# Performance work log

Hardware: AMD Instinct MI355X
Metric: run time of the kernel (lower is better)

Reference implementation:

```python
import jax, jax.numpy as jnp
import numpy as np

D_MODEL = 1024
D_STATE = 128
EXPAND = 2
HEADDIM = 64
D_CONV = 4
VAR_NUM = 3
D_INNER = EXPAND * D_MODEL            # 2048
NHEADS = D_INNER // HEADDIM           # 32
CONV_DIM = D_INNER + 2 * D_STATE      # 2304 (x, B, C share the conv)
D_IN_PROJ = 2 * D_INNER + 2 * D_STATE + NHEADS  # 4384


def setup_inputs() -> dict:
    key = jax.random.key(0)
    ks = jax.random.split(key, 10)
    s = 0.02
    B, L = 4, 2048
    return {
        "h_prev": jax.random.normal(ks[0], (B, L, D_MODEL), jnp.float32),
        "emb_next": jax.random.normal(ks[1], (B, L, D_MODEL), jnp.float32),
        "norm_w": jnp.ones((D_MODEL,), jnp.float32),
        "proj_W": jax.random.normal(ks[2], (D_MODEL, 2 * D_MODEL), jnp.float32) * s,
        "proj_b": jnp.zeros((D_MODEL,), jnp.float32),
        "in_proj_W": jax.random.normal(ks[3], (D_IN_PROJ, D_MODEL), jnp.float32) * s,
        "conv_w": jax.random.normal(ks[4], (CONV_DIM, D_CONV), jnp.float32) * s,
        "conv_b": jnp.zeros((CONV_DIM,), jnp.float32),
        "dt_bias": jax.random.uniform(ks[5], (NHEADS,), jnp.float32) * 0.1,
        "A_log": jnp.log(jnp.arange(1, NHEADS + 1, dtype=jnp.float32)),
        "D": jnp.ones((NHEADS,), jnp.float32),
        "gnorm_w": jnp.ones((D_INNER,), jnp.float32),
        "out_proj_W": jax.random.normal(ks[6], (D_MODEL, D_INNER), jnp.float32) * s,
        "dec_W": jax.random.normal(ks[7], (VAR_NUM, D_MODEL), jnp.float32) * s,
        "dec_b": jnp.zeros((VAR_NUM,), jnp.float32),
    }


def rmsnorm(x, w, eps=1e-6):
    xf = x.astype(jnp.float32)
    v = jnp.mean(jnp.square(xf), axis=-1, keepdims=True)
    return w * (xf * jax.lax.rsqrt(v + eps)).astype(x.dtype)


def gated_rmsnorm(y, z, w, eps=1e-5):
    y = y * jax.nn.silu(z)
    v = jnp.mean(jnp.square(y.astype(jnp.float32)), axis=-1, keepdims=True)
    return w * (y.astype(jnp.float32) * jax.lax.rsqrt(v + eps)).astype(y.dtype)


def mamba2(u, in_proj_W, conv_w, conv_b, dt_bias, A_log, D, gnorm_w, out_proj_W):
    B, L, _ = u.shape
    zxbcdt = u @ in_proj_W.T  # [B,L,D_IN_PROJ]
    z, xBC, dt = jnp.split(zxbcdt, [D_INNER, D_INNER + CONV_DIM], axis=-1)
    # causal depthwise conv over time
    lhs = jnp.moveaxis(xBC, -1, 1)               # [B,C,L]
    rhs = conv_w[:, None, :]                     # [C,1,K]
    conv = jax.lax.conv_general_dilated(lhs, rhs, (1,), [(D_CONV - 1, 0)],
                                        feature_group_count=CONV_DIM)
    xBC = jax.nn.silu(jnp.moveaxis(conv, 1, -1) + conv_b)
    x, Bm, Cm = jnp.split(xBC, [D_INNER, D_INNER + D_STATE], axis=-1)
    x = x.reshape(B, L, NHEADS, HEADDIM)         # [B,L,H,P]
    dt = jax.nn.softplus(dt + dt_bias)           # [B,L,H]
    A = -jnp.exp(A_log)                          # [H]
    dA = jnp.exp(dt * A)                         # [B,L,H]

    def step(state, inp):
        dA_t, dt_t, B_t, C_t, x_t = inp          # [B,H],[B,H],[B,N],[B,N],[B,H,P]
        state = state * dA_t[..., None, None] + (dt_t[..., None, None] * x_t[..., None]) * B_t[:, None, None, :]
        y_t = jnp.einsum('bhpn,bn->bhp', state, C_t)
        return state, y_t

    init = jnp.zeros((B, NHEADS, HEADDIM, D_STATE), u.dtype)
    xs = (jnp.moveaxis(dA, 1, 0), jnp.moveaxis(dt, 1, 0), jnp.moveaxis(Bm, 1, 0),
          jnp.moveaxis(Cm, 1, 0), jnp.moveaxis(x, 1, 0))
    _, y = jax.lax.scan(step, init, xs)          # y: [L,B,H,P]
    y = jnp.moveaxis(y, 0, 1) + D[None, None, :, None] * x
    y = y.reshape(B, L, D_INNER)
    y = gated_rmsnorm(y, z, gnorm_w)
    return y @ out_proj_W.T                      # [B,L,D_MODEL]


def reference(h_prev, emb_next, norm_w, proj_W, proj_b, in_proj_W, conv_w, conv_b,
              dt_bias, A_log, D, gnorm_w, out_proj_W, dec_W, dec_b):
    combined = jnp.concatenate([rmsnorm(h_prev, norm_w), rmsnorm(emb_next, norm_w)], axis=-1)
    h_prime = combined @ proj_W.T + proj_b       # [B,L,D_MODEL]
    h_k = mamba2(h_prime, in_proj_W, conv_w, conv_b, dt_bias, A_log, D, gnorm_w, out_proj_W)
    output = h_k @ dec_W.T + dec_b               # [B,L,VAR_NUM]
    return output, h_k
```

## Files before the change

kernel.cpp:

```cpp
#include <hip/hip_runtime.h>
#include <stdint.h>

#define T_TOK 8192
#define SEQL  2048
#define DM    1024
#define DI    2048
#define DSTATE 128
#define NH    32
#define HD    64
#define CONVD 2304
#define DINP  4384
#define LD_ZX 4480
#define QC    64
#define NCH   32

typedef __attribute__((ext_vector_type(8))) __bf16 bfrag;
typedef __attribute__((ext_vector_type(8))) short s16x8;
typedef __attribute__((ext_vector_type(4))) float f32x4;

__device__ __forceinline__ float bf2f(unsigned short u){
  return __uint_as_float(((unsigned)u) << 16);
}
__device__ __forceinline__ unsigned short f2bf(float f){
  unsigned u = __float_as_uint(f);
  unsigned r = (u + 0x7FFFu + ((u >> 16) & 1u)) >> 16;
  return (unsigned short)r;
}

__device__ __forceinline__ void gl_lds16(const unsigned short* g, unsigned short* l){
  __builtin_amdgcn_global_load_lds(
      (const __attribute__((address_space(1))) void*)g,
      (__attribute__((address_space(3))) void*)l,
      16, 0, 0);
}
__device__ __forceinline__ void gl_lds4(const float* g, float* l){
  __builtin_amdgcn_global_load_lds(
      (const __attribute__((address_space(1))) void*)g,
      (__attribute__((address_space(3))) void*)l,
      4, 0, 0);
}

__global__ __launch_bounds__(256) void cvt_w_kernel(const float* __restrict__ src,
                                                    unsigned short* __restrict__ dst,
                                                    int n4, int srcn4){
  int i = blockIdx.x * 256 + threadIdx.x;
  if (i >= n4) return;
  ushort4 o;
  if (i < srcn4){
    float4 v = ((const float4*)src)[i];
    o.x = f2bf(v.x); o.y = f2bf(v.y); o.z = f2bf(v.z); o.w = f2bf(v.w);
  } else {
    o.x = o.y = o.z = o.w = 0;
  }
  *(ushort4*)(dst + (size_t)i * 4) = o;
}

__global__ __launch_bounds__(256) void rmsnorm2_kernel(const float* __restrict__ a,
                                                       const float* __restrict__ b,
                                                       const float* __restrict__ w,
                                                       unsigned short* __restrict__ out){
  int t = blockIdx.x, tid = threadIdx.x;
  float4 va = *(const float4*)(a + (size_t)t * DM + tid * 4);
  float4 vb = *(const float4*)(b + (size_t)t * DM + tid * 4);
  float sa = va.x*va.x + va.y*va.y + va.z*va.z + va.w*va.w;
  float sb = vb.x*vb.x + vb.y*vb.y + vb.z*vb.z + vb.w*vb.w;
  #pragma unroll
  for (int o = 32; o; o >>= 1){ sa += __shfl_down(sa, o); sb += __shfl_down(sb, o); }
  __shared__ float reda[4], redb[4];
  int wv = tid >> 6, lane = tid & 63;
  if (!lane){ reda[wv] = sa; redb[wv] = sb; }
  __syncthreads();
  float ta = reda[0] + reda[1] + reda[2] + reda[3];
  float tb = redb[0] + redb[1] + redb[2] + redb[3];
  float ra = rsqrtf(ta * (1.f/1024.f) + 1e-6f);
  float rb = rsqrtf(tb * (1.f/1024.f) + 1e-6f);
  float4 vw = *(const float4*)(w + tid * 4);
  unsigned short* o0 = out + (size_t)t * DI + tid * 4;
  o0[0] = f2bf(va.x*ra*vw.x); o0[1] = f2bf(va.y*ra*vw.y);
  o0[2] = f2bf(va.z*ra*vw.z); o0[3] = f2bf(va.w*ra*vw.w);
  unsigned short* o1 = o0 + DM;
  o1[0] = f2bf(vb.x*rb*vw.x); o1[1] = f2bf(vb.y*rb*vw.y);
  o1[2] = f2bf(vb.z*rb*vw.z); o1[3] = f2bf(vb.w*rb*vw.w);
}

template<bool F32OUT>
__global__ __launch_bounds__(256) void gemm_bf16_kernel(const unsigned short* __restrict__ A,
                                                        const unsigned short* __restrict__ W,
                                                        void* __restrict__ Cv,
                                                        const float* __restrict__ bias,
                                                        int M, int N, int K, int ldc){
  __shared__ unsigned short As[128 * 64];
  __shared__ unsigned short Bs[128 * 64];
  const int nN = N >> 7;
  int bid = blockIdx.x;
  const int cpx = gridDim.x >> 3;
  bid = (bid & 7) * cpx + (bid >> 3);
  const int tm = bid / nN, tn = bid % nN;
  const int tid = threadIdx.x;
  const int wv = tid >> 6, lane = tid & 63;
  const int wm = wv >> 1, wn = wv & 1;
  const int rA = lane >> 3;
  const int cA = (lane & 7) << 3;
  const size_t arow0 = (size_t)(tm * 128) * K;
  const size_t brow0 = (size_t)(tn * 128) * K;

  f32x4 zero4 = {0.f, 0.f, 0.f, 0.f};
  f32x4 acc[4][4];
  #pragma unroll
  for (int i = 0; i < 4; ++i)
    #pragma unroll
    for (int j = 0; j < 4; ++j) acc[i][j] = zero4;

  const int nK = K >> 6;
  for (int kt = 0; kt < nK; ++kt){
    const int k0 = kt << 6;
    if (kt) __syncthreads();
    #pragma unroll
    for (int i = 0; i < 4; ++i){
      int base = (wv * 4 + i) * 8;
      gl_lds16(A + arow0 + (size_t)(base + rA) * K + k0 + cA, &As[base * 64]);
      gl_lds16(W + brow0 + (size_t)(base + rA) * K + k0 + cA, &Bs[base * 64]);
    }
    __syncthreads();
    #pragma unroll
    for (int kk = 0; kk < 2; ++kk){
      const int ko = kk * 32 + (lane >> 4) * 8;
      bfrag af[4], bfv[4];
      #pragma unroll
      for (int f = 0; f < 4; ++f){
        af[f]  = *reinterpret_cast<const bfrag*>(&As[(wm*64 + f*16 + (lane & 15)) * 64 + ko]);
        bfv[f] = *reinterpret_cast<const bfrag*>(&Bs[(wn*64 + f*16 + (lane & 15)) * 64 + ko]);
      }
      #pragma unroll
      for (int fm = 0; fm < 4; ++fm)
        #pragma unroll
        for (int fn = 0; fn < 4; ++fn)
          acc[fm][fn] = __builtin_amdgcn_mfma_f32_16x16x32_bf16(af[fm], bfv[fn], acc[fm][fn], 0, 0, 0);
    }
  }
  const int r0 = (lane >> 4) * 4, ci = lane & 15;
  #pragma unroll
  for (int fm = 0; fm < 4; ++fm){
    #pragma unroll
    for (int fn = 0; fn < 4; ++fn){
      int col = tn*128 + wn*64 + fn*16 + ci;
      float bv = bias ? bias[col] : 0.f;
      #pragma unroll
      for (int r = 0; r < 4; ++r){
        int row = tm*128 + wm*64 + fm*16 + r0 + r;
        float val = acc[fm][fn][r] + bv;
        if (F32OUT) ((float*)Cv)[(size_t)row * ldc + col] = val;
        else        ((unsigned short*)Cv)[(size_t)row * ldc + col] = f2bf(val);
      }
    }
  }
}

__global__ __launch_bounds__(256) void conv_kernel(const unsigned short* __restrict__ zx,
                                                   const float* __restrict__ cw,
                                                   const float* __restrict__ cb,
                                                   unsigned short* __restrict__ xbc){
  int c = blockIdx.x * 256 + threadIdx.x;
  int tg = blockIdx.y * 8;
  int l0 = tg & (SEQL - 1);
  const unsigned short* base = zx + (size_t)tg * LD_ZX + DI + c;
  float v[11];
  #pragma unroll
  for (int i = 0; i < 11; ++i){
    int ll = l0 - 3 + i;
    v[i] = (ll >= 0) ? bf2f(base[(ptrdiff_t)(i - 3) * LD_ZX]) : 0.f;
  }
  float w0 = cw[c*4+0], w1 = cw[c*4+1], w2 = cw[c*4+2], w3 = cw[c*4+3];
  float cbv = cb[c];
  unsigned short* ob = xbc + (size_t)tg * CONVD + c;
  #pragma unroll
  for (int s = 0; s < 8; ++s){
    float acc = cbv + w0*v[s] + w1*v[s+1] + w2*v[s+2] + w3*v[s+3];
    float sv = acc / (1.f + expf(-acc));
    ob[(size_t)s * CONVD] = f2bf(sv);
  }
}

__global__ __launch_bounds__(256) void cum_kernel(const unsigned short* __restrict__ zx,
                                                  const float* __restrict__ dtbias,
                                                  const float* __restrict__ alog,
                                                  float* __restrict__ cumT,
                                                  float* __restrict__ dtT,
                                                  float* __restrict__ decayG){
  int gw = blockIdx.x * 4 + (threadIdx.x >> 6);
  int l = threadIdx.x & 63;
  int c = gw & 31, h = (gw >> 5) & 31, b = gw >> 10;
  size_t t = (size_t)b * SEQL + c * QC + l;
  float xr = bf2f(zx[t * LD_ZX + 4352 + h]) + dtbias[h];
  float dt = (xr > 20.f) ? xr : log1pf(expf(xr));
  float A = -expf(alog[h]);
  float x = dt * A;
  #pragma unroll
  for (int d = 1; d < 64; d <<= 1){
    float y = __shfl_up(x, d);
    if (l >= d) x += y;
  }
  size_t o = ((size_t)(b * NH + h)) * SEQL + c * QC + l;
  cumT[o] = x;
  dtT[o] = dt;
  float tot = __shfl(x, 63);
  if (l == 0) decayG[(b * NH + h) * NCH + c] = expf(tot);
}

__global__ __launch_bounds__(256) void chunk_dS_kernel(const unsigned short* __restrict__ xbc,
                                                       const float* __restrict__ cumT,
                                                       const float* __restrict__ dtT,
                                                       unsigned short* __restrict__ dS){
  __shared__ unsigned short Xw[64 * 64];
  __shared__ unsigned short Bt[128 * 64];
  __shared__ float cumS[64], dtS[64];
  const int blk = blockIdx.x;
  const int c = blk & 31, h = (blk >> 5) & 31, b = blk >> 10;
  const int tid = threadIdx.x;
  const int wv = tid >> 6, l = tid & 63;
  const size_t tokB = (size_t)b * SEQL + c * QC;
  const int bh = b * NH + h;

  if (wv == 0) gl_lds4(cumT + (size_t)bh * SEQL + c * QC + l, cumS);
  if (wv == 1) gl_lds4(dtT  + (size_t)bh * SEQL + c * QC + l, dtS);

  const int j = tid >> 2, g4 = tid & 3;
  const unsigned short* xsrc = xbc + (tokB + j) * CONVD + h * HD + g4 * 16;
  s16x8 x0 = *(const s16x8*)xsrc, x1 = *(const s16x8*)(xsrc + 8);
  const unsigned short* bsrc = xbc + (tokB + j) * CONVD + DI + g4 * 32;
  s16x8 b0 = *(const s16x8*)bsrc,        b1 = *(const s16x8*)(bsrc + 8);
  s16x8 b2 = *(const s16x8*)(bsrc + 16), b3 = *(const s16x8*)(bsrc + 24);
  __syncthreads();

  float wj = expf(cumS[63] - cumS[j]) * dtS[j];
  const int jh = (j >> 3), jl = (j & 7);
  #pragma unroll
  for (int e = 0; e < 8; ++e){
    int p = g4 * 16 + e;
    Xw[p * 64 + ((jh ^ (p & 7)) << 3) + jl] = f2bf(bf2f((unsigned short)x0[e]) * wj);
    int p2 = p + 8;
    Xw[p2 * 64 + ((jh ^ (p2 & 7)) << 3) + jl] = f2bf(bf2f((unsigned short)x1[e]) * wj);
  }
  #pragma unroll
  for (int e = 0; e < 8; ++e){
    int n0 = g4 * 32 + e;
    Bt[(n0     ) * 64 + ((jh ^ ((n0     ) & 7)) << 3) + jl] = (unsigned short)b0[e];
    Bt[(n0 +  8) * 64 + ((jh ^ ((n0 +  8) & 7)) << 3) + jl] = (unsigned short)b1[e];
    Bt[(n0 + 16) * 64 + ((jh ^ ((n0 + 16) & 7)) << 3) + jl] = (unsigned short)b2[e];
    Bt[(n0 + 24) * 64 + ((jh ^ ((n0 + 24) & 7)) << 3) + jl] = (unsigned short)b3[e];
  }
  __syncthreads();

  f32x4 z4 = {0.f,0.f,0.f,0.f};
  f32x4 acc[4][2];
  #pragma unroll
  for (int pt = 0; pt < 4; ++pt){ acc[pt][0] = z4; acc[pt][1] = z4; }
  #pragma unroll
  for (int ks = 0; ks < 2; ++ks){
    const int au = ((ks * 4 + (l >> 4)) ^ (l & 7));
    bfrag a[4], bb[2];
    #pragma unroll
    for (int pt = 0; pt < 4; ++pt)
      a[pt] = *(const bfrag*)&Xw[(pt * 16 + (l & 15)) * 64 + au * 8];
    #pragma unroll
    for (int nt = 0; nt < 2; ++nt)
      bb[nt] = *(const bfrag*)&Bt[((wv * 2 + nt) * 16 + (l & 15)) * 64 + au * 8];
    #pragma unroll
    for (int pt = 0; pt < 4; ++pt)
      #pragma unroll
      for (int nt = 0; nt < 2; ++nt)
        acc[pt][nt] = __builtin_amdgcn_mfma_f32_16x16x32_bf16(a[pt], bb[nt], acc[pt][nt], 0, 0, 0);
  }
  unsigned short* out = dS + ((size_t)(bh * NCH + c) * 64) * 128;
  #pragma unroll
  for (int pt = 0; pt < 4; ++pt)
    #pragma unroll
    for (int nt = 0; nt < 2; ++nt)
      #pragma unroll
      for (int r = 0; r < 4; ++r){
        int p = pt * 16 + (l >> 4) * 4 + r;
        int n = (wv * 2 + nt) * 16 + (l & 15);
        out[(size_t)p * 128 + n] = f2bf(acc[pt][nt][r]);
      }
}

__global__ __launch_bounds__(256) void chunk_state_kernel(const float* __restrict__ decayG,
                                                          unsigned short* __restrict__ dS){
  int i = blockIdx.x * 256 + threadIdx.x;
  int n = i & 127, p = (i >> 7) & 63, bh = i >> 13;
  float s = 0.f;
  #pragma unroll 4
  for (int c = 0; c < NCH; ++c){
    size_t idx = ((size_t)(bh * NCH + c) * 64 + p) * 128 + n;
    unsigned short d = dS[idx];
    dS[idx] = f2bf(s);
    s = decayG[bh * NCH + c] * s + bf2f(d);
  }
}

__global__ __launch_bounds__(256) void chunk_Y_kernel(const unsigned short* __restrict__ xbc,
                                                      const unsigned short* __restrict__ Sb,
                                                      const float* __restrict__ cumT,
                                                      const float* __restrict__ dtT,
                                                      const float* __restrict__ Dvec,
                                                      unsigned short* __restrict__ ybuf){
  __shared__ unsigned short Cs[64 * 128];
  __shared__ unsigned short Bs[64 * 128];
  __shared__ unsigned short Xt[64 * 64];
  __shared__ unsigned short Ms[64 * 64];
  __shared__ float cumS[64], dtS[64];
  const int blk = blockIdx.x;
  const int c = blk & 31, h = (blk >> 5) & 31, b = blk >> 10;
  const int tid = threadIdx.x;
  const int wv = tid >> 6, l = tid & 63;
  const size_t tokB = (size_t)b * SEQL + c * QC;
  const int bh = b * NH + h;

  #pragma unroll
  for (int kk = 0; kk < 4; ++kk){
    int k = wv * 4 + kk;
    int row = k * 4 + (l >> 4);
    int us = (l & 15) ^ (row & 7);
    gl_lds16(xbc + (tokB + row) * CONVD + 2176 + us * 8, &Cs[k * 512]);
    gl_lds16(xbc + (tokB + row) * CONVD + 2048 + us * 8, &Bs[k * 512]);
  }
  if (wv == 0) gl_lds4(cumT + (size_t)bh * SEQL + c * QC + l, cumS);
  if (wv == 1) gl_lds4(dtT  + (size_t)bh * SEQL + c * QC + l, dtS);

  {
    const int j = tid >> 2, g4 = tid & 3;
    const unsigned short* xsrc = xbc + (tokB + j) * CONVD + h * HD + g4 * 16;
    s16x8 x0 = *(const s16x8*)xsrc, x1 = *(const s16x8*)(xsrc + 8);
    const int jh = j >> 3, jl = j & 7;
    #pragma unroll
    for (int e = 0; e < 8; ++e){
      int p = g4 * 16 + e;
      Xt[p * 64 + ((jh ^ (p & 7)) << 3) + jl] = (unsigned short)x0[e];
      int p2 = p + 8;
      Xt[p2 * 64 + ((jh ^ (p2 & 7)) << 3) + jl] = (unsigned short)x1[e];
    }
  }
  __syncthreads();

  bfrag sbf[4][4];
  {
    const unsigned short* sbase = Sb + (size_t)(bh * NCH + c) * 64 * 128;
    #pragma unroll
    for (int pt = 0; pt < 4; ++pt)
      #pragma unroll
      for (int ks = 0; ks < 4; ++ks){
        int p = pt * 16 + (l & 15);
        sbf[pt][ks] = *(const bfrag*)(sbase + (size_t)p * 128 + ks * 32 + (l >> 4) * 8);
      }
  }

  f32x4 z4 = {0.f,0.f,0.f,0.f};
  f32x4 macc[4] = {z4, z4, z4, z4};
  #pragma unroll
  for (int ks = 0; ks < 4; ++ks){
    const int au = (ks * 4 + (l >> 4)) ^ (l & 7);
    bfrag ca = *(const bfrag*)&Cs[(wv * 16 + (l & 15)) * 128 + au * 8];
    #pragma unroll
    for (int jt = 0; jt < 4; ++jt){
      bfrag bb = *(const bfrag*)&Bs[(jt * 16 + (l & 15)) * 128 + au * 8];
      macc[jt] = __builtin_amdgcn_mfma_f32_16x16x32_bf16(ca, bb, macc[jt], 0, 0, 0);
    }
  }
  float cj[4], dj[4];
  #pragma unroll
  for (int jt = 0; jt < 4; ++jt){
    int jv = jt * 16 + (l & 15);
    cj[jt] = cumS[jv]; dj[jt] = dtS[jv];
  }
  float ctv[4];
  #pragma unroll
  for (int r = 0; r < 4; ++r) ctv[r] = cumS[wv * 16 + (l >> 4) * 4 + r];
  #pragma unroll
  for (int jt = 0; jt < 4; ++jt){
    int jv = jt * 16 + (l & 15);
    #pragma unroll
    for (int r = 0; r < 4; ++r){
      int tb = wv * 16 + (l >> 4) * 4 + r;
      float g = (jv <= tb) ? expf(ctv[r] - cj[jt]) * dj[jt] : 0.f;
      Ms[tb * 64 + (((jv >> 3) ^ (tb & 7)) << 3) + (jv & 7)] = f2bf(macc[jt][r] * g);
    }
  }
  f32x4 yacc[4] = {z4, z4, z4, z4};
  #pragma unroll
  for (int kj = 0; kj < 2; ++kj){
    const int au = (kj * 4 + (l >> 4)) ^ (l & 7);
    bfrag ma = *(const bfrag*)&Ms[(wv * 16 + (l & 15)) * 64 + au * 8];
    #pragma unroll
    for (int pt = 0; pt < 4; ++pt){
      bfrag wx = *(const bfrag*)&Xt[(pt * 16 + (l & 15)) * 64 + au * 8];
      yacc[pt] = __builtin_amdgcn_mfma_f32_16x16x32_bf16(ma, wx, yacc[pt], 0, 0, 0);
    }
  }
  f32x4 iacc[4] = {z4, z4, z4, z4};
  #pragma unroll
  for (int ks = 0; ks < 4; ++ks){
    const int au = (ks * 4 + (l >> 4)) ^ (l & 7);
    bfrag ca = *(const bfrag*)&Cs[(wv * 16 + (l & 15)) * 128 + au * 8];
    #pragma unroll
    for (int pt = 0; pt < 4; ++pt)
      iacc[pt] = __builtin_amdgcn_mfma_f32_16x16x32_bf16(ca, sbf[pt][ks], iacc[pt], 0, 0, 0);
  }
  const float Dh = Dvec[h];
  float er[4];
  #pragma unroll
  for (int r = 0; r < 4; ++r) er[r] = expf(ctv[r]);
  #pragma unroll
  for (int pt = 0; pt < 4; ++pt)
    #pragma unroll
    for (int r = 0; r < 4; ++r){
      int p = pt * 16 + (l & 15);
      int tb = wv * 16 + (l >> 4) * 4 + r;
      float xv = bf2f(Xt[p * 64 + (((tb >> 3) ^ (p & 7)) << 3) + (tb & 7)]);
      float yv = yacc[pt][r] + er[r] * iacc[pt][r] + Dh * xv;
      ybuf[(tokB + tb) * DI + h * HD + p] = f2bf(yv);
    }
}

__global__ __launch_bounds__(256) void gated_kernel(const unsigned short* __restrict__ y,
                                                    const unsigned short* __restrict__ zx,
                                                    const float* __restrict__ gw,
                                                    unsigned short* __restrict__ out){
  int t = blockIdx.x, tid = threadIdx.x;
  s16x8 yv = *(const s16x8*)(y  + (size_t)t * DI    + tid * 8);
  s16x8 zv = *(const s16x8*)(zx + (size_t)t * LD_ZX + tid * 8);
  float g[8]; float ss = 0.f;
  #pragma unroll
  for (int j = 0; j < 8; ++j){
    float yf = bf2f((unsigned short)yv[j]);
    float zf = bf2f((unsigned short)zv[j]);
    float gi = yf * (zf / (1.f + expf(-zf)));
    g[j] = gi; ss += gi * gi;
  }
  #pragma unroll
  for (int o = 32; o; o >>= 1) ss += __shfl_down(ss, o);
  __shared__ float red[4];
  int wv = tid >> 6, lane = tid & 63;
  if (!lane) red[wv] = ss;
  __syncthreads();
  float tot = red[0] + red[1] + red[2] + red[3];
  float sc = rsqrtf(tot * (1.f/2048.f) + 1e-5f);
  unsigned short* o0 = out + (size_t)t * DI + tid * 8;
  #pragma unroll
  for (int j = 0; j < 8; ++j) o0[j] = f2bf(g[j] * sc * gw[tid * 8 + j]);
}

__global__ __launch_bounds__(256) void dec_kernel(const float* __restrict__ hk,
                                                  const float* __restrict__ dw,
                                                  const float* __restrict__ db,
                                                  float* __restrict__ out){
  int t = (blockIdx.x * 256 + threadIdx.x) >> 6;
  int lane = threadIdx.x & 63;
  const float* hr = hk + (size_t)t * DM + lane * 16;
  float h[16];
  #pragma unroll
  for (int j = 0; j < 16; ++j) h[j] = hr[j];
  float a0 = 0.f, a1 = 0.f, a2 = 0.f;
  const float* w0 = dw + lane * 16;
  const float* w1 = dw + DM + lane * 16;
  const float* w2 = dw + 2 * DM + lane * 16;
  #pragma unroll
  for (int j = 0; j < 16; ++j){
    a0 = fmaf(h[j], w0[j], a0);
    a1 = fmaf(h[j], w1[j], a1);
    a2 = fmaf(h[j], w2[j], a2);
  }
  #pragma unroll
  for (int o = 32; o; o >>= 1){
    a0 += __shfl_down(a0, o);
    a1 += __shfl_down(a1, o);
    a2 += __shfl_down(a2, o);
  }
  if (!lane){
    out[t * 3 + 0] = a0 + db[0];
    out[t * 3 + 1] = a1 + db[1];
    out[t * 3 + 2] = a2 + db[2];
  }
}

extern "C" void kernel_launch(void* const* d_in, const int* in_sizes, int n_in,
                              void* d_out, int out_size, void* d_ws, size_t ws_size,
                              hipStream_t stream){
  const float* h_prev    = (const float*)d_in[0];
  const float* emb_next  = (const float*)d_in[1];
  const float* norm_w    = (const float*)d_in[2];
  const float* proj_W    = (const float*)d_in[3];
  const float* proj_b    = (const float*)d_in[4];
  const float* in_proj_W = (const float*)d_in[5];
  const float* conv_w    = (const float*)d_in[6];
  const float* conv_b    = (const float*)d_in[7];
  const float* dt_bias   = (const float*)d_in[8];
  const float* A_log     = (const float*)d_in[9];
  const float* Dvec      = (const float*)d_in[10];
  const float* gnorm_w   = (const float*)d_in[11];
  const float* out_proj_W= (const float*)d_in[12];
  const float* dec_W     = (const float*)d_in[13];
  const float* dec_b     = (const float*)d_in[14];

  char* ws = (char*)d_ws;
  size_t off = 0;
  auto take = [&](size_t bytes){ char* p = ws + off; off += (bytes + 255) & ~(size_t)255; return p; };
  unsigned short* wproj = (unsigned short*)take((size_t)DM * DI * 2);
  unsigned short* winp  = (unsigned short*)take((size_t)LD_ZX * DM * 2);
  unsigned short* wout  = (unsigned short*)take((size_t)DM * DI * 2);
  unsigned short* zx    = (unsigned short*)take((size_t)T_TOK * LD_ZX * 2);
  float*          cumT  = (float*)take((size_t)4 * NH * SEQL * 4);
  float*          dtT   = (float*)take((size_t)4 * NH * SEQL * 4);
  float*          decayG= (float*)take((size_t)4 * NH * NCH * 4);
  char* regionA = take((size_t)T_TOK * CONVD * 2);
  unsigned short* combined = (unsigned short*)regionA;
  unsigned short* xbc      = (unsigned short*)regionA;
  char* regionY = take((size_t)T_TOK * DI * 2);
  unsigned short* hprime = (unsigned short*)regionY;
  unsigned short* ybuf   = (unsigned short*)regionY;
  unsigned short* dS = (unsigned short*)take((size_t)128 * NCH * 64 * 128 * 2);

  float* outp = (float*)d_out;
  float* hk   = outp + (size_t)T_TOK * 3;

  cvt_w_kernel<<<2048, 256, 0, stream>>>(proj_W, wproj, DM*DI/4, DM*DI/4);
  cvt_w_kernel<<<4480, 256, 0, stream>>>(in_proj_W, winp, LD_ZX*DM/4, DINP*DM/4);
  cvt_w_kernel<<<2048, 256, 0, stream>>>(out_proj_W, wout, DM*DI/4, DM*DI/4);

  rmsnorm2_kernel<<<T_TOK, 256, 0, stream>>>(h_prev, emb_next, norm_w, combined);

  gemm_bf16_kernel<false><<<(T_TOK/128)*(DM/128), 256, 0, stream>>>(combined, wproj, hprime, proj_b,
                                                                    T_TOK, DM, DI, DM);
  gemm_bf16_kernel<false><<<(T_TOK/128)*(LD_ZX/128), 256, 0, stream>>>(hprime, winp, zx, nullptr,
                                                                       T_TOK, LD_ZX, DM, LD_ZX);
  conv_kernel<<<dim3(CONVD/256, T_TOK/8), 256, 0, stream>>>(zx, conv_w, conv_b, xbc);
  cum_kernel<<<1024, 256, 0, stream>>>(zx, dt_bias, A_log, cumT, dtT, decayG);
  chunk_dS_kernel<<<4096, 256, 0, stream>>>(xbc, cumT, dtT, dS);
  chunk_state_kernel<<<4096, 256, 0, stream>>>(decayG, dS);
  chunk_Y_kernel<<<4096, 256, 0, stream>>>(xbc, dS, cumT, dtT, Dvec, ybuf);
  gated_kernel<<<T_TOK, 256, 0, stream>>>(ybuf, zx, gnorm_w, ybuf);
  gemm_bf16_kernel<true><<<(T_TOK/128)*(DM/128), 256, 0, stream>>>(ybuf, wout, hk, nullptr,
                                                                   T_TOK, DM, DI, DM);
  dec_kernel<<<T_TOK/4, 256, 0, stream>>>(hk, dec_W, dec_b, outp);
}
```

Baseline: 402.0 us.

## Merge weight conversions, widen conv time tile, vectorize chunk state scan

The three weight-conversion launches are merged into one kernel that picks its source by block index, saving two launches. The conv kernel now handles 16 timesteps per thread instead of 8, so the 3-step halo reload is a smaller share of its loads. The inter-chunk state recurrence handles 8 state elements per thread with 16-byte vector loads and stores, replacing scalar 2-byte accesses. The catch is that chunk_state launches 8x fewer threads (512 blocks), so less parallelism is available to hide the serial per-chunk latency.

```diff
diff --git a/kernel.cpp b/kernel.cpp
--- a/kernel.cpp
+++ b/kernel.cpp
@@ -40,11 +40,21 @@
       4, 0, 0);
 }
 
-__global__ __launch_bounds__(256) void cvt_w_kernel(const float* __restrict__ src,
-                                                    unsigned short* __restrict__ dst,
-                                                    int n4, int srcn4){
-  int i = blockIdx.x * 256 + threadIdx.x;
-  if (i >= n4) return;
+__global__ __launch_bounds__(256) void cvt_all_kernel(const float* __restrict__ s0,
+                                                      const float* __restrict__ s1,
+                                                      const float* __restrict__ s2,
+                                                      unsigned short* __restrict__ d0,
+                                                      unsigned short* __restrict__ d1,
+                                                      unsigned short* __restrict__ d2){
+  int blk = blockIdx.x;
+  const float* src; unsigned short* dst; int i, srcn4;
+  if (blk < 2048){
+    src = s0; dst = d0; i = blk * 256 + threadIdx.x; srcn4 = DM * DI / 4;
+  } else if (blk < 6528){
+    src = s1; dst = d1; i = (blk - 2048) * 256 + threadIdx.x; srcn4 = DINP * DM / 4;
+  } else {
+    src = s2; dst = d2; i = (blk - 6528) * 256 + threadIdx.x; srcn4 = DM * DI / 4;
+  }
   ushort4 o;
   if (i < srcn4){
     float4 v = ((const float4*)src)[i];
@@ -161,12 +171,12 @@
                                                    const float* __restrict__ cb,
                                                    unsigned short* __restrict__ xbc){
   int c = blockIdx.x * 256 + threadIdx.x;
-  int tg = blockIdx.y * 8;
+  int tg = blockIdx.y * 16;
   int l0 = tg & (SEQL - 1);
   const unsigned short* base = zx + (size_t)tg * LD_ZX + DI + c;
-  float v[11];
-  #pragma unroll
-  for (int i = 0; i < 11; ++i){
+  float v[19];
+  #pragma unroll
+  for (int i = 0; i < 19; ++i){
     int ll = l0 - 3 + i;
     v[i] = (ll >= 0) ? bf2f(base[(ptrdiff_t)(i - 3) * LD_ZX]) : 0.f;
   }
@@ -174,7 +184,7 @@
   float cbv = cb[c];
   unsigned short* ob = xbc + (size_t)tg * CONVD + c;
   #pragma unroll
-  for (int s = 0; s < 8; ++s){
+  for (int s = 0; s < 16; ++s){
     float acc = cbv + w0*v[s] + w1*v[s+1] + w2*v[s+2] + w3*v[s+3];
     float sv = acc / (1.f + expf(-acc));
     ob[(size_t)s * CONVD] = f2bf(sv);
@@ -287,14 +297,21 @@
 __global__ __launch_bounds__(256) void chunk_state_kernel(const float* __restrict__ decayG,
                                                           unsigned short* __restrict__ dS){
   int i = blockIdx.x * 256 + threadIdx.x;
-  int n = i & 127, p = (i >> 7) & 63, bh = i >> 13;
-  float s = 0.f;
-  #pragma unroll 4
+  int n8 = i & 15, p = (i >> 4) & 63, bh = i >> 10;
+  float s[8];
+  #pragma unroll
+  for (int j = 0; j < 8; ++j) s[j] = 0.f;
+  const float* dg = decayG + bh * NCH;
   for (int c = 0; c < NCH; ++c){
-    size_t idx = ((size_t)(bh * NCH + c) * 64 + p) * 128 + n;
-    unsigned short d = dS[idx];
-    dS[idx] = f2bf(s);
-    s = decayG[bh * NCH + c] * s + bf2f(d);
+    size_t idx = ((size_t)(bh * NCH + c) * 64 + p) * 128 + n8 * 8;
+    s16x8 d = *(const s16x8*)(dS + idx);
+    s16x8 o;
+    #pragma unroll
+    for (int j = 0; j < 8; ++j) o[j] = (short)f2bf(s[j]);
+    *(s16x8*)(dS + idx) = o;
+    float g = dg[c];
+    #pragma unroll
+    for (int j = 0; j < 8; ++j) s[j] = fmaf(g, s[j], bf2f((unsigned short)d[j]));
   }
 }
 
@@ -522,9 +539,8 @@
   float* outp = (float*)d_out;
   float* hk   = outp + (size_t)T_TOK * 3;
 
-  cvt_w_kernel<<<2048, 256, 0, stream>>>(proj_W, wproj, DM*DI/4, DM*DI/4);
-  cvt_w_kernel<<<4480, 256, 0, stream>>>(in_proj_W, winp, LD_ZX*DM/4, DINP*DM/4);
-  cvt_w_kernel<<<2048, 256, 0, stream>>>(out_proj_W, wout, DM*DI/4, DM*DI/4);
+  cvt_all_kernel<<<8576, 256, 0, stream>>>(proj_W, in_proj_W, out_proj_W,
+                                           wproj, winp, wout);
 
   rmsnorm2_kernel<<<T_TOK, 256, 0, stream>>>(h_prev, emb_next, norm_w, combined);
 
@@ -532,10 +548,10 @@
                                                                     T_TOK, DM, DI, DM);
   gemm_bf16_kernel<false><<<(T_TOK/128)*(LD_ZX/128), 256, 0, stream>>>(hprime, winp, zx, nullptr,
                                                                        T_TOK, LD_ZX, DM, LD_ZX);
-  conv_kernel<<<dim3(CONVD/256, T_TOK/8), 256, 0, stream>>>(zx, conv_w, conv_b, xbc);
+  conv_kernel<<<dim3(CONVD/256, T_TOK/16), 256, 0, stream>>>(zx, conv_w, conv_b, xbc);
   cum_kernel<<<1024, 256, 0, stream>>>(zx, dt_bias, A_log, cumT, dtT, decayG);
   chunk_dS_kernel<<<4096, 256, 0, stream>>>(xbc, cumT, dtT, dS);
-  chunk_state_kernel<<<4096, 256, 0, stream>>>(decayG, dS);
+  chunk_state_kernel<<<512, 256, 0, stream>>>(decayG, dS);
   chunk_Y_kernel<<<4096, 256, 0, stream>>>(xbc, dS, cumT, dtT, Dvec, ybuf);
   gated_kernel<<<T_TOK, 256, 0, stream>>>(ybuf, zx, gnorm_w, ybuf);
   gemm_bf16_kernel<true><<<(T_TOK/128)*(DM/128), 256, 0, stream>>>(ybuf, wout, hk, nullptr,
```

Result: faster. 392.5 us (-2.3%).
